# Kernel optimization log

Measured on AMD Instinct MI355X. Metric: run time of the kernel, lower is better.

Reference implementation:

```python
import jax, jax.numpy as jnp
import numpy as np

B, L, HID, NH = 1, 2048, 3072, 24
HD = HID // NH          # 128
MLP = HID * 4           # 12288


def _layernorm(x, eps=1e-6):
    # LayerNorm without affine (pre_norm)
    mu = jnp.mean(x, axis=-1, keepdims=True)
    var = jnp.mean(jnp.square(x - mu), axis=-1, keepdims=True)
    return (x - mu) * jax.lax.rsqrt(var + eps)


def _rmsnorm(x, w):
    # torch.nn.RMSNorm with eps=None -> finfo(dtype).eps
    eps = jnp.finfo(x.dtype).eps
    ms = jnp.mean(jnp.square(x), axis=-1, keepdims=True)
    return x * jax.lax.rsqrt(ms + eps) * w


def _apply_rope(x, pe):
    # x: (B, L, H, D); pe: (B, 1, L, D//2, 2, 2)
    b, l, h, d = x.shape
    x_ = x.astype(jnp.float32).reshape(b, l, h, d // 2, 1, 2)
    f = pe[:, :, :, None]                       # (B,1,L,1,D//2,2,2)
    out = f[..., 0] * x_[..., 0] + f[..., 1] * x_[..., 1]
    return out.reshape(b, l, h, d).astype(x.dtype)


def setup_inputs() -> dict:
    key = jax.random.key(0)
    ks = jax.random.split(key, 16)
    s = 0.02
    # pe as proper 2x2 rotation matrices (EmbedND output structure)
    theta = jax.random.uniform(ks[0], (L, HD // 2), minval=0.0, maxval=2.0 * np.pi)
    cos, sin = jnp.cos(theta), jnp.sin(theta)
    rot = jnp.stack([jnp.stack([cos, -sin], -1), jnp.stack([sin, cos], -1)], -2)
    pe = rot[None, None].astype(jnp.float32)    # (1,1,L,HD//2,2,2)
    rnd = lambda k, shp: jax.random.normal(k, shp, jnp.float32)
    return {
        "x": rnd(ks[1], (B, L, HID)),
        "vec": rnd(ks[2], (B, HID)),
        "pe": pe,
        "w_mod": rnd(ks[3], (HID, 3 * HID)) * s,
        "b_mod": rnd(ks[4], (3 * HID,)) * s,
        "w_qkv": rnd(ks[5], (HID, 3 * HID)) * s,
        "b_qkv": rnd(ks[6], (3 * HID,)) * s,
        "w_fc1": rnd(ks[7], (HID, MLP)) * s,
        "b_fc1": rnd(ks[8], (MLP,)) * s,
        "w_fc2": rnd(ks[9], (MLP, HID)) * s,
        "b_fc2": rnd(ks[10], (HID,)) * s,
        "w_out": rnd(ks[11], (HID, HID)) * s,
        "b_out": rnd(ks[12], (HID,)) * s,
        "norm_q_w": jnp.ones((HD,), jnp.float32),
        "norm_k_w": jnp.ones((HD,), jnp.float32),
    }


def reference(x, vec, pe, w_mod, b_mod, w_qkv, b_qkv, w_fc1, b_fc1,
              w_fc2, b_fc2, w_out, b_out, norm_q_w, norm_k_w):
    # modulation: AWQ linear on silu(vec)
    mod = jax.nn.silu(vec) @ w_mod + b_mod            # (B, 3*HID)
    shift, scale, gate = jnp.split(mod[:, None, :], 3, axis=-1)
    x_mod = _layernorm(x) * (1.0 + scale) + shift      # (B, L, HID)

    # qkv projection (SVDQ linear, dequantized math == dense GEMM)
    qkv = x_mod @ w_qkv + b_qkv
    q, k, v = jnp.split(qkv, 3, axis=-1)
    q = _rmsnorm(q.reshape(B, L, NH, HD), norm_q_w)
    k = _rmsnorm(k.reshape(B, L, NH, HD), norm_k_w)
    q = _apply_rope(q, pe)
    k = _apply_rope(k, pe)
    v = v.reshape(B, L, NH, HD)

    # scaled dot-product attention
    scores = jnp.einsum("blhd,bmhd->bhlm", q, k) / jnp.sqrt(jnp.float32(HD))
    probs = jax.nn.softmax(scores, axis=-1)
    attn = jnp.einsum("bhlm,bmhd->blhd", probs, v).reshape(B, L, HID)

    # parallel MLP branch
    mlp = jax.nn.gelu(x_mod @ w_fc1 + b_fc1, approximate=True)
    mlp = mlp @ w_fc2 + b_fc2

    out = attn @ w_out + b_out + mlp
    return x + gate * out
```

## Files before the change

kernel.cpp:

```cpp
#include <hip/hip_runtime.h>
#include <hip/hip_bf16.h>
#include <stdint.h>


typedef __bf16 bf16;
typedef bf16 bf16x2 __attribute__((ext_vector_type(2)));
typedef bf16 bf16x4 __attribute__((ext_vector_type(4)));
typedef bf16 bf16x8 __attribute__((ext_vector_type(8)));
typedef float f32x4 __attribute__((ext_vector_type(4)));

#define L_SEQ 2048
#define HIDD  3072
#define NHH   24
#define HDD   128
#define MLPD  12288
#define N3Q   9216

struct PB { bf16* p[8]; };

__device__ __forceinline__ void gload_lds16(const bf16* g, bf16* l) {
  __builtin_amdgcn_global_load_lds(
      (const __attribute__((address_space(1))) unsigned int*)g,
      (__attribute__((address_space(3))) unsigned int*)l, 16, 0, 0);
}

__device__ __forceinline__ float gelu_tanh(float x) {
  float z = 0.7978845608028654f * (x + 0.044715f * x * x * x);
  float t = 1.f - 2.f / (__expf(2.f * z) + 1.f);
  return 0.5f * x * (1.f + t);
}

__global__ __launch_bounds__(256) void mod_partial(
    const float* __restrict__ vec, const float* __restrict__ w_mod,
    float* __restrict__ part) {
  __shared__ float sv[256];
  int y = blockIdx.y;
  int i0 = y * 256;
  {
    float xv = vec[i0 + threadIdx.x];
    sv[threadIdx.x] = xv / (1.f + __expf(-xv));
  }
  __syncthreads();
  int j = blockIdx.x * 256 + threadIdx.x;
  float acc = 0.f;
#pragma unroll 8
  for (int i = 0; i < 256; ++i)
    acc += sv[i] * w_mod[(size_t)(i0 + i) * N3Q + j];
  part[y * N3Q + j] = acc;
}

__global__ __launch_bounds__(256) void mod_reduce(
    const float* __restrict__ part, const float* __restrict__ b_mod,
    float* __restrict__ mod) {
  int j = blockIdx.x * 256 + threadIdx.x;
  float s = b_mod[j];
#pragma unroll
  for (int p = 0; p < 12; ++p) s += part[p * N3Q + j];
  mod[j] = s;
}

__global__ __launch_bounds__(256) void ln_mod_k(
    const float* __restrict__ x, const float* __restrict__ mod,
    bf16* __restrict__ xm) {
  __shared__ float sb[4];
  int l = blockIdx.x, t = threadIdx.x;
  const float* xr = x + (size_t)l * HIDD;
  float4 v[3];
  float s = 0.f;
#pragma unroll
  for (int p = 0; p < 3; ++p) {
    v[p] = *(const float4*)(xr + p * 1024 + t * 4);
    s += v[p].x + v[p].y + v[p].z + v[p].w;
  }
#pragma unroll
  for (int o = 32; o >= 1; o >>= 1) s += __shfl_xor(s, o);
  if (!(t & 63)) sb[t >> 6] = s;
  __syncthreads();
  float mean = (sb[0] + sb[1] + sb[2] + sb[3]) * (1.f / HIDD);
  __syncthreads();
  float vs = 0.f;
#pragma unroll
  for (int p = 0; p < 3; ++p) {
    float a = v[p].x - mean, b = v[p].y - mean, c = v[p].z - mean,
          d = v[p].w - mean;
    vs += a * a + b * b + c * c + d * d;
  }
#pragma unroll
  for (int o = 32; o >= 1; o >>= 1) vs += __shfl_xor(vs, o);
  if (!(t & 63)) sb[t >> 6] = vs;
  __syncthreads();
  float var = (sb[0] + sb[1] + sb[2] + sb[3]) * (1.f / HIDD);
  float rs = rsqrtf(var + 1e-6f);
#pragma unroll
  for (int p = 0; p < 3; ++p) {
    int j = p * 1024 + t * 4;
    float4 sc = *(const float4*)(mod + HIDD + j);
    float4 sh = *(const float4*)(mod + j);
    bf16x4 o;
    o[0] = (bf16)((v[p].x - mean) * rs * (1.f + sc.x) + sh.x);
    o[1] = (bf16)((v[p].y - mean) * rs * (1.f + sc.y) + sh.y);
    o[2] = (bf16)((v[p].z - mean) * rs * (1.f + sc.z) + sh.z);
    o[3] = (bf16)((v[p].w - mean) * rs * (1.f + sc.w) + sh.w);
    *(bf16x4*)(xm + (size_t)l * HIDD + j) = o;
  }
}

__global__ __launch_bounds__(256) void convT(
    const float* __restrict__ src, bf16* __restrict__ dst, int K, int N) {
  __shared__ bf16 tl[64 * 72];
  int n0 = blockIdx.x * 64, k0 = blockIdx.y * 64;
  int t = threadIdx.x;
#pragma unroll
  for (int p = 0; p < 4; ++p) {
    int idx = p * 256 + t;
    int kr = idx >> 4, c4 = (idx & 15) << 2;
    float4 v = *(const float4*)(src + (size_t)(k0 + kr) * N + n0 + c4);
    bf16x4 b;
    b[0] = (bf16)v.x; b[1] = (bf16)v.y; b[2] = (bf16)v.z; b[3] = (bf16)v.w;
    *(bf16x4*)(tl + kr * 72 + c4) = b;
  }
  __syncthreads();
#pragma unroll
  for (int p = 0; p < 2; ++p) {
    int idx = p * 256 + t;
    int nr = idx >> 3, c = idx & 7;
    bf16x8 o;
#pragma unroll
    for (int j = 0; j < 8; ++j) o[j] = tl[(c * 8 + j) * 72 + nr];
    *(bf16x8*)(dst + (size_t)(n0 + nr) * K + k0 + c * 8) = o;
  }
}

template <int EPI>
__global__ __launch_bounds__(512, 2) void gemm256(
    const bf16* __restrict__ A, const bf16* __restrict__ BT,
    const float* __restrict__ bias, int lda, int klen, int ldc, int gy,
    int gz, PB dst, bf16* __restrict__ o1) {
  __shared__ bf16 LA[2][2][8192];
  __shared__ bf16 LB[2][2][8192];
  const int tid = threadIdx.x;
  const int w = tid >> 6, lane = tid & 63;
  const int wm = w >> 2, wn = w & 3;
  const int g = lane >> 4, r16 = lane & 15;
  const int hb = wn >> 1, brow = (wn & 1) * 64;

  const int nwg = 8 * gy * gz;
  int id = (int)blockIdx.x;
  int sw = (id & 7) * (nwg >> 3) + (id >> 3);
  const int bx = sw & 7;
  const int rem = sw >> 3;
  const int by = rem % gy;
  const int bz = rem / gy;

  const int row0 = bx * 256, col0 = by * 256;
  const size_t kb = (size_t)bz * klen;

  const int s_r = tid >> 3, s_c = tid & 7;
  const bf16* gA = A + (size_t)(row0 + s_r) * lda + kb + ((s_c ^ (s_r & 7)) << 3);
  const bf16* gB = BT + (size_t)(col0 + s_r) * lda + kb + ((s_c ^ (s_r & 7)) << 3);
  const int wofs = w * 512;

#define STG_A(buf, h, t)                                                       \
  do {                                                                         \
    gload_lds16(gA + (size_t)((h) * 128) * lda + (size_t)(t) * 64,             \
                &LA[buf][h][wofs]);                                            \
    gload_lds16(gA + (size_t)((h) * 128 + 64) * lda + (size_t)(t) * 64,        \
                &LA[buf][h][4096 + wofs]);                                     \
  } while (0)
#define STG_B(buf, h, t)                                                       \
  do {                                                                         \
    gload_lds16(gB + (size_t)((h) * 128) * lda + (size_t)(t) * 64,             \
                &LB[buf][h][wofs]);                                            \
    gload_lds16(gB + (size_t)((h) * 128 + 64) * lda + (size_t)(t) * 64,        \
                &LB[buf][h][4096 + wofs]);                                     \
  } while (0)
#define LGKM0()                                               \
  do {                                                        \
    asm volatile("s_waitcnt lgkmcnt(0)" ::: "memory");        \
    __builtin_amdgcn_sched_barrier(0);                        \
  } while (0)
#define RD_A4(DST, LAP, MB)                                                    \
  _Pragma("unroll") for (int m_ = 0; m_ < 4; ++m_)                             \
  _Pragma("unroll") for (int kk_ = 0; kk_ < 2; ++kk_)                          \
      DST[m_][kk_] = *(const bf16x8*)((LAP) + (((MB) + m_) * 16 + r16) * 64 +  \
                                      (((kk_ * 4 + g) ^ (r16 & 7)) << 3));
#define RD_B2(DST, LBP, NB)                                                    \
  _Pragma("unroll") for (int n_ = 0; n_ < 2; ++n_)                             \
  _Pragma("unroll") for (int kk_ = 0; kk_ < 2; ++kk_)                          \
      DST[n_][kk_] = *(const bf16x8*)(                                         \
          (LBP) + (brow + ((NB) + n_) * 16 + r16) * 64 +                       \
          (((kk_ * 4 + g) ^ (r16 & 7)) << 3));
#define QUAD(AF, BF, MB, NB)                                                   \
  do {                                                                         \
    __builtin_amdgcn_s_setprio(1);                                             \
    _Pragma("unroll") for (int kk_ = 0; kk_ < 2; ++kk_)                        \
    _Pragma("unroll") for (int m_ = 0; m_ < 4; ++m_)                           \
    _Pragma("unroll") for (int n_ = 0; n_ < 2; ++n_)                           \
        acc[(MB) + m_][(NB) + n_] = __builtin_amdgcn_mfma_f32_16x16x32_bf16(   \
            AF[m_][kk_], BF[n_][kk_], acc[(MB) + m_][(NB) + n_], 0, 0, 0);     \
    __builtin_amdgcn_s_setprio(0);                                             \
  } while (0)

#define GROUP(TB, T1, T2)                                                      \
  do {                                                                         \
    const bf16* la = &LA[TB][wm][0];                                           \
    const bf16* lb = &LB[TB][hb][0];                                           \
    bf16x8 aL[4][2], aH[4][2], bL[2][2], bH[2][2];                             \
                                           \
    RD_A4(aL, la, 0);                                                          \
    RD_B2(bL, lb, 0);                                                          \
    if ((T1) < nk) STG_B(TB ^ 1, 1, T1);                                       \
    asm volatile("s_waitcnt lgkmcnt(8)" ::: "memory");                         \
    __builtin_amdgcn_s_barrier();                                              \
    LGKM0();                                                                   \
    QUAD(aL, bL, 0, 0);                                                        \
    __builtin_amdgcn_s_barrier();                                              \
                      \
    RD_A4(aH, la, 4);                                                          \
    __builtin_amdgcn_s_barrier();                                              \
    LGKM0();                                                                   \
    QUAD(aH, bL, 4, 0);                                                        \
    __builtin_amdgcn_s_barrier();                                              \
     \
    RD_B2(bH, lb, 2);                                                          \
    if ((T2) < nk) { STG_A(TB, 0, T2); STG_A(TB, 1, T2); }                     \
    __builtin_amdgcn_s_barrier();                                              \
    LGKM0();                                                                   \
    QUAD(aL, bH, 0, 2);                                                        \
    __builtin_amdgcn_s_barrier();                                              \
       \
    if ((T2) < nk) {                                                           \
      STG_B(TB, 0, T2);                                                        \
      asm volatile("s_waitcnt vmcnt(6)" ::: "memory");                         \
    } else {                                                                   \
      asm volatile("s_waitcnt vmcnt(0)" ::: "memory");                         \
    }                                                                          \
    __builtin_amdgcn_s_barrier();                                              \
    QUAD(aH, bH, 4, 2);                                                        \
    __builtin_amdgcn_s_barrier();                                              \
  } while (0)

  f32x4 acc[8][4] = {};
  const int nk = klen >> 6;

  STG_A(0, 0, 0); STG_A(0, 1, 0); STG_B(0, 0, 0); STG_B(0, 1, 0);
  STG_A(1, 0, 1); STG_A(1, 1, 1); STG_B(1, 0, 1);
  asm volatile("s_waitcnt vmcnt(6)" ::: "memory");
  __builtin_amdgcn_s_barrier();

  for (int t = 0; t < nk; t += 2) {
    GROUP(0, t + 1, t + 2);
    GROUP(1, t + 2, t + 3);
  }
#undef STG_A
#undef STG_B
#undef LGKM0
#undef RD_A4
#undef RD_B2
#undef QUAD
#undef GROUP

  bf16* dp = (EPI == 0) ? dst.p[bz] : o1;
#pragma unroll
  for (int m = 0; m < 8; ++m) {
    int row = row0 + wm * 128 + m * 16 + g * 4;
#pragma unroll
    for (int n = 0; n < 4; ++n) {
      int col = col0 + wn * 64 + n * 16 + r16;
      float bv = (EPI == 1) ? bias[col] : 0.f;
#pragma unroll
      for (int r = 0; r < 4; ++r) {
        float v = acc[m][n][r] + bv;
        if (EPI == 1) v = gelu_tanh(v);
        dp[(size_t)(row + r) * ldc + col] = (bf16)v;
      }
    }
  }
}

__global__ __launch_bounds__(256) void qknorm_rope_k(
    const bf16* __restrict__ P0, const bf16* __restrict__ P1,
    const float* __restrict__ b_qkv, const float* __restrict__ pe,
    const float* __restrict__ qw, const float* __restrict__ kw,
    bf16* __restrict__ qb, bf16* __restrict__ kb) {
  int t = threadIdx.x, lane = t & 63, w = t >> 6;
  int pair = blockIdx.x * 4 + w;
  int h = pair % NHH, l = pair / NHH;
  size_t qi = (size_t)l * N3Q + h * HDD + 2 * lane;
  size_t ob = (size_t)l * HIDD + h * HDD + 2 * lane;
  float4 f = *(const float4*)(pe + (size_t)l * 256 + lane * 4);
  float2 wq = *(const float2*)(qw + 2 * lane);
  float2 wk = *(const float2*)(kw + 2 * lane);
  {
    bf16x2 a = *(const bf16x2*)(P0 + qi);
    bf16x2 b = *(const bf16x2*)(P1 + qi);
    float2 bq = *(const float2*)(b_qkv + h * HDD + 2 * lane);
    float x0 = (float)a[0] + (float)b[0] + bq.x;
    float x1 = (float)a[1] + (float)b[1] + bq.y;
    float ss = x0 * x0 + x1 * x1;
#pragma unroll
    for (int o = 32; o >= 1; o >>= 1) ss += __shfl_xor(ss, o);
    float rs = rsqrtf(ss * (1.f / HDD) + 1.1920929e-7f);
    x0 *= rs * wq.x; x1 *= rs * wq.y;
    const float qs = 0.08838834764831845f;
    bf16x2 ov;
    ov[0] = (bf16)((f.x * x0 + f.y * x1) * qs);
    ov[1] = (bf16)((f.z * x0 + f.w * x1) * qs);
    *(bf16x2*)(qb + ob) = ov;
  }
  {
    bf16x2 a = *(const bf16x2*)(P0 + qi + HIDD);
    bf16x2 b = *(const bf16x2*)(P1 + qi + HIDD);
    float2 bk = *(const float2*)(b_qkv + HIDD + h * HDD + 2 * lane);
    float x0 = (float)a[0] + (float)b[0] + bk.x;
    float x1 = (float)a[1] + (float)b[1] + bk.y;
    float ss = x0 * x0 + x1 * x1;
#pragma unroll
    for (int o = 32; o >= 1; o >>= 1) ss += __shfl_xor(ss, o);
    float rs = rsqrtf(ss * (1.f / HDD) + 1.1920929e-7f);
    x0 *= rs * wk.x; x1 *= rs * wk.y;
    bf16x2 ov;
    ov[0] = (bf16)(f.x * x0 + f.y * x1);
    ov[1] = (bf16)(f.z * x0 + f.w * x1);
    *(bf16x2*)(kb + ob) = ov;
  }
}

__global__ __launch_bounds__(256) void vtrans_k(
    const bf16* __restrict__ P0, const bf16* __restrict__ P1,
    const float* __restrict__ b_qkv, bf16* __restrict__ vt) {
  __shared__ bf16 tl[128 * 128];
  int t = threadIdx.x, lt = blockIdx.x, h = blockIdx.y;
#pragma unroll
  for (int p = 0; p < 8; ++p) {
    int idx = p * 256 + t;
    int i = idx >> 4, c = idx & 15;
    size_t gi = (size_t)(lt * 128 + i) * N3Q + 2 * HIDD + h * HDD + c * 8;
    bf16x8 a = *(const bf16x8*)(P0 + gi);
    bf16x8 b = *(const bf16x8*)(P1 + gi);
    bf16x8 val;
#pragma unroll
    for (int e = 0; e < 8; ++e)
      val[e] = (bf16)((float)a[e] + (float)b[e] +
                      b_qkv[2 * HIDD + h * HDD + c * 8 + e]);
    *(bf16x8*)(tl + i * 128 + ((c ^ (i & 15)) << 3)) = val;
  }
  __syncthreads();
#pragma unroll
  for (int p = 0; p < 8; ++p) {
    int idx = p * 256 + t;
    int j = idx >> 4, i8 = (idx & 15) << 3;
    bf16x8 o;
#pragma unroll
    for (int e = 0; e < 8; ++e) {
      int row = i8 + e;
      o[e] = tl[row * 128 + ((((j >> 3) ^ (row & 15)) << 3) | (j & 7))];
    }
    *(bf16x8*)(vt + ((size_t)h * HDD + j) * L_SEQ + lt * 128 + i8) = o;
  }
}

__global__ __launch_bounds__(256) void attn_k(
    const bf16* __restrict__ q, const bf16* __restrict__ k,
    const bf16* __restrict__ vt, bf16* __restrict__ out) {
  __shared__ bf16 Ks[64 * 128];
  __shared__ bf16 Vs[128 * 64];
  __shared__ bf16 Ps[4][16 * 72];
  int tid = threadIdx.x, lane = tid & 63, w = tid >> 6;
  int g = lane >> 4, r16 = lane & 15;
  int qt = blockIdx.x, h = blockIdx.y;
  int qbase = qt * 64 + w * 16;

  bf16x8 qreg[4];
  const bf16* qrow = q + (size_t)(qbase + r16) * HIDD + h * HDD;
#pragma unroll
  for (int c = 0; c < 4; ++c) qreg[c] = *(const bf16x8*)(qrow + c * 32 + g * 8);

  f32x4 acc[8] = {};
  float m_run = -3.0e38f, l_run = 0.f;
  bf16* ps = &Ps[w][0];

  for (int kv0 = 0; kv0 < L_SEQ; kv0 += 64) {
    __syncthreads();
#pragma unroll
    for (int p = 0; p < 4; ++p) {
      int ci = p * 256 + tid;
      {
        int rr = ci >> 4, cc = ci & 15;
        gload_lds16(k + (size_t)(kv0 + rr) * HIDD + h * HDD +
                        ((cc ^ (rr & 15)) << 3),
                    Ks + ((p * 4 + w) << 9));
      }
      {
        int rr = ci >> 3, cc = ci & 7;
        gload_lds16(vt + ((size_t)h * HDD + rr) * L_SEQ + kv0 +
                        ((cc ^ (rr & 7)) << 3),
                    Vs + ((p * 4 + w) << 9));
      }
    }
    __syncthreads();

    f32x4 st[4] = {};
#pragma unroll
    for (int m4 = 0; m4 < 4; ++m4) {
#pragma unroll
      for (int c = 0; c < 4; ++c) {
        int rr = m4 * 16 + r16;
        bf16x8 kf =
            *(const bf16x8*)(Ks + rr * 128 + (((c * 4 + g) ^ (rr & 15)) << 3));
        st[m4] =
            __builtin_amdgcn_mfma_f32_16x16x32_bf16(kf, qreg[c], st[m4], 0, 0, 0);
      }
    }
    float cmax = -3.0e38f;
#pragma unroll
    for (int m4 = 0; m4 < 4; ++m4)
#pragma unroll
      for (int r = 0; r < 4; ++r) cmax = fmaxf(cmax, st[m4][r]);
    cmax = fmaxf(cmax, __shfl_xor(cmax, 16));
    cmax = fmaxf(cmax, __shfl_xor(cmax, 32));
    float m_new = fmaxf(m_run, cmax);
    float corr = __expf(m_run - m_new);
    float psum = 0.f;
#pragma unroll
    for (int m4 = 0; m4 < 4; ++m4) {
      bf16x4 pk;
#pragma unroll
      for (int r = 0; r < 4; ++r) {
        float pv = __expf(st[m4][r] - m_new);
        psum += pv;
        pk[r] = (bf16)pv;
      }
      *(bf16x4*)(ps + r16 * 72 + m4 * 16 + g * 4) = pk;
    }
    psum += __shfl_xor(psum, 16);
    psum += __shfl_xor(psum, 32);
    l_run = l_run * corr + psum;
    m_run = m_new;
    float corr_r[4];
#pragma unroll
    for (int r = 0; r < 4; ++r) corr_r[r] = __shfl(corr, g * 4 + r);
#pragma unroll
    for (int nt = 0; nt < 8; ++nt)
#pragma unroll
      for (int r = 0; r < 4; ++r) acc[nt][r] *= corr_r[r];
#pragma unroll
    for (int ks = 0; ks < 2; ++ks) {
      bf16x8 pf = *(const bf16x8*)(ps + r16 * 72 + ks * 32 + g * 8);
#pragma unroll
      for (int nt = 0; nt < 8; ++nt) {
        int rr = nt * 16 + r16;
        bf16x8 vf =
            *(const bf16x8*)(Vs + rr * 64 + (((ks * 4 + g) ^ (rr & 7)) << 3));
        acc[nt] = __builtin_amdgcn_mfma_f32_16x16x32_bf16(pf, vf, acc[nt], 0, 0, 0);
      }
    }
  }
  float inv = 1.f / l_run;
  float inv_r[4];
#pragma unroll
  for (int r = 0; r < 4; ++r) inv_r[r] = __shfl(inv, g * 4 + r);
#pragma unroll
  for (int nt = 0; nt < 8; ++nt)
#pragma unroll
    for (int r = 0; r < 4; ++r)
      out[(size_t)(qbase + g * 4 + r) * HIDD + h * HDD + nt * 16 + r16] =
          (bf16)(acc[nt][r] * inv_r[r]);
}

__global__ __launch_bounds__(256) void osum_k(
    const bf16* __restrict__ a, const bf16* __restrict__ b,
    const bf16* __restrict__ c, const bf16* __restrict__ d,
    float* __restrict__ o) {
  size_t i = ((size_t)blockIdx.x * 256 + threadIdx.x) * 4;
  bf16x4 va = *(const bf16x4*)(a + i);
  bf16x4 vb = *(const bf16x4*)(b + i);
  bf16x4 vc = *(const bf16x4*)(c + i);
  bf16x4 vd = *(const bf16x4*)(d + i);
  float4 s;
  s.x = (float)va[0] + (float)vb[0] + (float)vc[0] + (float)vd[0];
  s.y = (float)va[1] + (float)vb[1] + (float)vc[1] + (float)vd[1];
  s.z = (float)va[2] + (float)vb[2] + (float)vc[2] + (float)vd[2];
  s.w = (float)va[3] + (float)vb[3] + (float)vc[3] + (float)vd[3];
  *(float4*)(o + i) = s;
}

__global__ __launch_bounds__(256) void final_k(
    const float* __restrict__ x, PB ps, const float* __restrict__ mod,
    const float* __restrict__ b_out, const float* __restrict__ b_fc2,
    float* __restrict__ out) {
  int l = blockIdx.x, t = threadIdx.x;
#pragma unroll
  for (int p = 0; p < 3; ++p) {
    int c = p * 1024 + t * 4;
    size_t idx = (size_t)l * HIDD + c;
    float4 xv = *(const float4*)(x + idx);
    float4 gv = *(const float4*)(mod + 2 * HIDD + c);
    float4 bo = *(const float4*)(b_out + c);
    float4 bf = *(const float4*)(b_fc2 + c);
    float4 da = *(const float4*)(out + idx);
    float a0 = da.x + bo.x + bf.x, a1 = da.y + bo.y + bf.y;
    float a2 = da.z + bo.z + bf.z, a3 = da.w + bo.w + bf.w;
#pragma unroll
    for (int i = 0; i < 8; ++i) {
      bf16x4 v = *(const bf16x4*)(ps.p[i] + idx);
      a0 += (float)v[0]; a1 += (float)v[1];
      a2 += (float)v[2]; a3 += (float)v[3];
    }
    float4 o;
    o.x = xv.x + gv.x * a0;
    o.y = xv.y + gv.y * a1;
    o.z = xv.z + gv.z * a2;
    o.w = xv.w + gv.w * a3;
    *(float4*)(out + idx) = o;
  }
}

extern "C" void kernel_launch(void* const* d_in, const int* in_sizes, int n_in,
                              void* d_out, int out_size, void* d_ws,
                              size_t ws_size, hipStream_t stream) {
  const float* x     = (const float*)d_in[0];
  const float* vec   = (const float*)d_in[1];
  const float* pe    = (const float*)d_in[2];
  const float* w_mod = (const float*)d_in[3];
  const float* b_mod = (const float*)d_in[4];
  const float* w_qkv = (const float*)d_in[5];
  const float* b_qkv = (const float*)d_in[6];
  const float* w_fc1 = (const float*)d_in[7];
  const float* b_fc1 = (const float*)d_in[8];
  const float* w_fc2 = (const float*)d_in[9];
  const float* b_fc2 = (const float*)d_in[10];
  const float* w_out = (const float*)d_in[11];
  const float* b_out = (const float*)d_in[12];
  const float* qw    = (const float*)d_in[13];
  const float* kw    = (const float*)d_in[14];
  float* out = (float*)d_out;

  char* ws = (char*)d_ws;
  float* mod  = (float*)(ws + 0);
  bf16* xmod  = (bf16*)(ws + 65536);
  bf16* qb    = (bf16*)(ws + 12648448);
  bf16* kbuf  = (bf16*)(ws + 25231360);
  bf16* vt    = (bf16*)(ws + 37814272);
  bf16* att   = (bf16*)(ws + 50397184);
  bf16* mlpF  = (bf16*)(ws + 62980096);
  bf16* wt    = (bf16*)(ws + 113311744);
  bf16* P0    = (bf16*)(ws + 188809216);
  float* part = (float*)(ws + 188809216);
  bf16* P1    = mlpF;
  bf16* H1    = (bf16*)(ws + 188809216 + 12582912);
  bf16* H2    = (bf16*)(ws + 188809216 + 25165824);
  PB Z = {};

  mod_partial<<<dim3(36, 12), 256, 0, stream>>>(vec, w_mod, part);
  mod_reduce<<<36, 256, 0, stream>>>(part, b_mod, mod);
  ln_mod_k<<<2048, 256, 0, stream>>>(x, mod, xmod);

  convT<<<dim3(144, 48), 256, 0, stream>>>(w_qkv, wt, 3072, 9216);
  PB Pq = {}; Pq.p[0] = P0; Pq.p[1] = P1;
  gemm256<0><<<576, 512, 0, stream>>>(xmod, wt, nullptr, 3072, 1536, 9216, 36,
                                      2, Pq, nullptr);
  qknorm_rope_k<<<12288, 256, 0, stream>>>(P0, P1, b_qkv, pe, qw, kw, qb, kbuf);
  vtrans_k<<<dim3(16, 24), 256, 0, stream>>>(P0, P1, b_qkv, vt);
  attn_k<<<dim3(32, 24), 256, 0, stream>>>(qb, kbuf, vt, att);

  convT<<<dim3(48, 48), 256, 0, stream>>>(w_out, wt, 3072, 3072);
  PB Po = {}; Po.p[0] = qb; Po.p[1] = kbuf; Po.p[2] = vt; Po.p[3] = P0;
  gemm256<0><<<384, 512, 0, stream>>>(att, wt, nullptr, 3072, 768, 3072, 12, 4,
                                      Po, nullptr);
  osum_k<<<6144, 256, 0, stream>>>(qb, kbuf, vt, P0, out);

  convT<<<dim3(192, 48), 256, 0, stream>>>(w_fc1, wt, 3072, 12288);
  gemm256<1><<<384, 512, 0, stream>>>(xmod, wt, b_fc1, 3072, 3072, 12288, 48,
                                      1, Z, mlpF);

  convT<<<dim3(48, 192), 256, 0, stream>>>(w_fc2, wt, 12288, 3072);
  PB Pf = {};
  Pf.p[0] = xmod; Pf.p[1] = qb; Pf.p[2] = kbuf; Pf.p[3] = vt;
  Pf.p[4] = att;  Pf.p[5] = P0; Pf.p[6] = H1;   Pf.p[7] = H2;
  gemm256<0><<<768, 512, 0, stream>>>(mlpF, wt, nullptr, 12288, 1536, 3072, 12,
                                      8, Pf, nullptr);

  final_k<<<2048, 256, 0, stream>>>(x, Pf, mod, b_out, b_fc2, out);
}
```

Baseline: 876.2 us.

## Software-pipeline LDS fragment reads in GEMM and split-K the fc1 GEMM

Restructures the GEMM inner GROUP so that each fragment's LDS reads are issued one quad ahead, including prefetching the next tile's A-low fragment, and drops several barriers and lgkm waits. The goal is to hide LDS latency behind MFMA work. Separately, fc1 now runs as a 2-way split-K GEMM writing bf16 partials, followed by a new elementwise kernel that sums the partials, adds the bias and applies GELU. This doubles the grid to fill the GPU, at the cost of extra partial-buffer traffic, one more launch, and bf16 rounding of the partials before the sum.

```diff
diff --git a/kernel.cpp b/kernel.cpp
--- a/kernel.cpp
+++ b/kernel.cpp
@@ -179,6 +179,7 @@
     asm volatile("s_waitcnt lgkmcnt(0)" ::: "memory");        \
     __builtin_amdgcn_sched_barrier(0);                        \
   } while (0)
+#define SB0() __builtin_amdgcn_sched_barrier(0)
 #define RD_A4(DST, LAP, MB)                                                    \
   _Pragma("unroll") for (int m_ = 0; m_ < 4; ++m_)                             \
   _Pragma("unroll") for (int kk_ = 0; kk_ < 2; ++kk_)                          \
@@ -205,48 +206,50 @@
   do {                                                                         \
     const bf16* la = &LA[TB][wm][0];                                           \
     const bf16* lb = &LB[TB][hb][0];                                           \
-    bf16x8 aL[4][2], aH[4][2], bL[2][2], bH[2][2];                             \
-                                           \
-    RD_A4(aL, la, 0);                                                          \
+    const bf16* laN = &LA[TB ^ 1][wm][0];                                      \
+          \
+    LGKM0();                                                                   \
+    if ((T1) < nk) STG_B(TB ^ 1, 1, T1);                                       \
     RD_B2(bL, lb, 0);                                                          \
-    if ((T1) < nk) STG_B(TB ^ 1, 1, T1);                                       \
-    asm volatile("s_waitcnt lgkmcnt(8)" ::: "memory");                         \
-    __builtin_amdgcn_s_barrier();                                              \
-    LGKM0();                                                                   \
+    RD_A4(aH, la, 4);                                                          \
+    SB0();                                                                     \
     QUAD(aL, bL, 0, 0);                                                        \
     __builtin_amdgcn_s_barrier();                                              \
-                      \
-    RD_A4(aH, la, 4);                                                          \
-    __builtin_amdgcn_s_barrier();                                              \
+                                               \
     LGKM0();                                                                   \
+    RD_B2(bH, lb, 2);                                                          \
+    SB0();                                                                     \
     QUAD(aH, bL, 4, 0);                                                        \
     __builtin_amdgcn_s_barrier();                                              \
-     \
-    RD_B2(bH, lb, 2);                                                          \
-    if ((T2) < nk) { STG_A(TB, 0, T2); STG_A(TB, 1, T2); }                     \
-    __builtin_amdgcn_s_barrier();                                              \
+         \
     LGKM0();                                                                   \
-    QUAD(aL, bH, 0, 2);                                                        \
-    __builtin_amdgcn_s_barrier();                                              \
-       \
     if ((T2) < nk) {                                                           \
-      STG_B(TB, 0, T2);                                                        \
-      asm volatile("s_waitcnt vmcnt(6)" ::: "memory");                         \
+      STG_A(TB, 0, T2);                                                        \
+      STG_A(TB, 1, T2);                                                        \
+      asm volatile("s_waitcnt vmcnt(4)" ::: "memory");                         \
     } else {                                                                   \
       asm volatile("s_waitcnt vmcnt(0)" ::: "memory");                         \
     }                                                                          \
+    SB0();                                                                     \
+    QUAD(aL, bH, 0, 2);                                                        \
     __builtin_amdgcn_s_barrier();                                              \
+          \
+    if ((T2) < nk) STG_B(TB, 0, T2);                                           \
+    if ((T1) < nk) { RD_A4(aL, laN, 0); }                                      \
+    SB0();                                                                     \
     QUAD(aH, bH, 4, 2);                                                        \
     __builtin_amdgcn_s_barrier();                                              \
   } while (0)
 
   f32x4 acc[8][4] = {};
+  bf16x8 aL[4][2], aH[4][2], bL[2][2], bH[2][2];
   const int nk = klen >> 6;
 
   STG_A(0, 0, 0); STG_A(0, 1, 0); STG_B(0, 0, 0); STG_B(0, 1, 0);
   STG_A(1, 0, 1); STG_A(1, 1, 1); STG_B(1, 0, 1);
   asm volatile("s_waitcnt vmcnt(6)" ::: "memory");
   __builtin_amdgcn_s_barrier();
+  { const bf16* la0 = &LA[0][wm][0]; RD_A4(aL, la0, 0); }
 
   for (int t = 0; t < nk; t += 2) {
     GROUP(0, t + 1, t + 2);
@@ -255,6 +258,7 @@
 #undef STG_A
 #undef STG_B
 #undef LGKM0
+#undef SB0
 #undef RD_A4
 #undef RD_B2
 #undef QUAD
@@ -485,6 +489,23 @@
   *(float4*)(o + i) = s;
 }
 
+__global__ __launch_bounds__(256) void sumgelu_k(
+    const bf16* __restrict__ p0, const bf16* __restrict__ p1,
+    const float* __restrict__ b, bf16* __restrict__ o) {
+  size_t i = ((size_t)blockIdx.x * 256 + threadIdx.x) * 8;
+  int col = (int)(i % MLPD);
+  bf16x8 a = *(const bf16x8*)(p0 + i);
+  bf16x8 c = *(const bf16x8*)(p1 + i);
+  float4 b0 = *(const float4*)(b + col);
+  float4 b1 = *(const float4*)(b + col + 4);
+  float bb[8] = {b0.x, b0.y, b0.z, b0.w, b1.x, b1.y, b1.z, b1.w};
+  bf16x8 o8;
+#pragma unroll
+  for (int j = 0; j < 8; ++j)
+    o8[j] = (bf16)gelu_tanh((float)a[j] + (float)c[j] + bb[j]);
+  *(bf16x8*)(o + i) = o8;
+}
+
 __global__ __launch_bounds__(256) void final_k(
     const float* __restrict__ x, PB ps, const float* __restrict__ mod,
     const float* __restrict__ b_out, const float* __restrict__ b_fc2,
@@ -571,8 +592,10 @@
   osum_k<<<6144, 256, 0, stream>>>(qb, kbuf, vt, P0, out);
 
   convT<<<dim3(192, 48), 256, 0, stream>>>(w_fc1, wt, 3072, 12288);
-  gemm256<1><<<384, 512, 0, stream>>>(xmod, wt, b_fc1, 3072, 3072, 12288, 48,
-                                      1, Z, mlpF);
+  PB Pg = {}; Pg.p[0] = mlpF; Pg.p[1] = qb;
+  gemm256<0><<<768, 512, 0, stream>>>(xmod, wt, nullptr, 3072, 1536, 12288, 48,
+                                      2, Pg, nullptr);
+  sumgelu_k<<<12288, 256, 0, stream>>>(mlpF, qb, b_fc1, mlpF);
 
   convT<<<dim3(48, 192), 256, 0, stream>>>(w_fc2, wt, 12288, 3072);
   PB Pf = {};
```

New measurement: 1.136 ms. 1.3x slower.

## Fuse QKV and FC1 GEMMs into one launch without split-K

Applied to the files above, without the earlier changes.

Merges the QKV projection and the FC1+GELU projection, which share the same xmod input, into a single GEMM launch over a concatenated output width. Each tile picks its transposed weight source and epilogue based on its column block. The QKV part no longer uses split-K, so qknorm and vtrans read one partial buffer instead of summing two. Transposed weights are staged in reused scratch (the q buffer and the output buffer), which ties correctness to buffer lifetimes and gives a larger single grid with full-K tiles.

```diff
diff --git a/kernel.cpp b/kernel.cpp
--- a/kernel.cpp
+++ b/kernel.cpp
@@ -135,7 +135,8 @@
 __global__ __launch_bounds__(512, 2) void gemm256(
     const bf16* __restrict__ A, const bf16* __restrict__ BT,
     const float* __restrict__ bias, int lda, int klen, int ldc, int gy,
-    int gz, PB dst, bf16* __restrict__ o1) {
+    int gz, PB dst, const bf16* __restrict__ BT2,
+    const bf16* __restrict__ BT3) {
   __shared__ bf16 LA[2][2][8192];
   __shared__ bf16 LB[2][2][8192];
   const int tid = threadIdx.x;
@@ -157,7 +158,14 @@
 
   const int s_r = tid >> 3, s_c = tid & 7;
   const bf16* gA = A + (size_t)(row0 + s_r) * lda + kb + ((s_c ^ (s_r & 7)) << 3);
-  const bf16* gB = BT + (size_t)(col0 + s_r) * lda + kb + ((s_c ^ (s_r & 7)) << 3);
+  const bf16* bbase = BT;
+  int bcol = col0;
+  if (EPI == 2) {
+    if (by >= 36)      { bbase = BT3; bcol = col0 - 9216; }
+    else if (by >= 32) { bbase = BT2; bcol = col0 - 8192; }
+  }
+  const bf16* gB =
+      bbase + (size_t)(bcol + s_r) * lda + kb + ((s_c ^ (s_r & 7)) << 3);
   const int wofs = w * 512;
 
 #define STG_A(buf, h, t)                                                       \
@@ -260,29 +268,54 @@
 #undef QUAD
 #undef GROUP
 
-  bf16* dp = (EPI == 0) ? dst.p[bz] : o1;
-#pragma unroll
-  for (int m = 0; m < 8; ++m) {
-    int row = row0 + wm * 128 + m * 16 + g * 4;
-#pragma unroll
-    for (int n = 0; n < 4; ++n) {
-      int col = col0 + wn * 64 + n * 16 + r16;
-      float bv = (EPI == 1) ? bias[col] : 0.f;
-#pragma unroll
-      for (int r = 0; r < 4; ++r) {
-        float v = acc[m][n][r] + bv;
-        if (EPI == 1) v = gelu_tanh(v);
-        dp[(size_t)(row + r) * ldc + col] = (bf16)v;
+  if (EPI == 2 && by < 36) {
+    bf16* dp = dst.p[0];
+#pragma unroll
+    for (int m = 0; m < 8; ++m) {
+      int row = row0 + wm * 128 + m * 16 + g * 4;
+#pragma unroll
+      for (int n = 0; n < 4; ++n) {
+        int col = col0 + wn * 64 + n * 16 + r16;
+#pragma unroll
+        for (int r = 0; r < 4; ++r)
+          dp[(size_t)(row + r) * N3Q + col] = (bf16)acc[m][n][r];
+      }
+    }
+  } else if (EPI == 2) {
+    bf16* dp = dst.p[1];
+#pragma unroll
+    for (int m = 0; m < 8; ++m) {
+      int row = row0 + wm * 128 + m * 16 + g * 4;
+#pragma unroll
+      for (int n = 0; n < 4; ++n) {
+        int col = col0 - 9216 + wn * 64 + n * 16 + r16;
+        float bv = bias[col];
+#pragma unroll
+        for (int r = 0; r < 4; ++r)
+          dp[(size_t)(row + r) * MLPD + col] = (bf16)gelu_tanh(acc[m][n][r] + bv);
+      }
+    }
+  } else {
+    bf16* dp = dst.p[bz];
+#pragma unroll
+    for (int m = 0; m < 8; ++m) {
+      int row = row0 + wm * 128 + m * 16 + g * 4;
+#pragma unroll
+      for (int n = 0; n < 4; ++n) {
+        int col = col0 + wn * 64 + n * 16 + r16;
+#pragma unroll
+        for (int r = 0; r < 4; ++r)
+          dp[(size_t)(row + r) * ldc + col] = (bf16)acc[m][n][r];
       }
     }
   }
 }
 
 __global__ __launch_bounds__(256) void qknorm_rope_k(
-    const bf16* __restrict__ P0, const bf16* __restrict__ P1,
-    const float* __restrict__ b_qkv, const float* __restrict__ pe,
-    const float* __restrict__ qw, const float* __restrict__ kw,
-    bf16* __restrict__ qb, bf16* __restrict__ kb) {
+    const bf16* __restrict__ P, const float* __restrict__ b_qkv,
+    const float* __restrict__ pe, const float* __restrict__ qw,
+    const float* __restrict__ kw, bf16* __restrict__ qb,
+    bf16* __restrict__ kb) {
   int t = threadIdx.x, lane = t & 63, w = t >> 6;
   int pair = blockIdx.x * 4 + w;
   int h = pair % NHH, l = pair / NHH;
@@ -292,11 +325,10 @@
   float2 wq = *(const float2*)(qw + 2 * lane);
   float2 wk = *(const float2*)(kw + 2 * lane);
   {
-    bf16x2 a = *(const bf16x2*)(P0 + qi);
-    bf16x2 b = *(const bf16x2*)(P1 + qi);
+    bf16x2 a = *(const bf16x2*)(P + qi);
     float2 bq = *(const float2*)(b_qkv + h * HDD + 2 * lane);
-    float x0 = (float)a[0] + (float)b[0] + bq.x;
-    float x1 = (float)a[1] + (float)b[1] + bq.y;
+    float x0 = (float)a[0] + bq.x;
+    float x1 = (float)a[1] + bq.y;
     float ss = x0 * x0 + x1 * x1;
 #pragma unroll
     for (int o = 32; o >= 1; o >>= 1) ss += __shfl_xor(ss, o);
@@ -309,11 +341,10 @@
     *(bf16x2*)(qb + ob) = ov;
   }
   {
-    bf16x2 a = *(const bf16x2*)(P0 + qi + HIDD);
-    bf16x2 b = *(const bf16x2*)(P1 + qi + HIDD);
+    bf16x2 a = *(const bf16x2*)(P + qi + HIDD);
     float2 bk = *(const float2*)(b_qkv + HIDD + h * HDD + 2 * lane);
-    float x0 = (float)a[0] + (float)b[0] + bk.x;
-    float x1 = (float)a[1] + (float)b[1] + bk.y;
+    float x0 = (float)a[0] + bk.x;
+    float x1 = (float)a[1] + bk.y;
     float ss = x0 * x0 + x1 * x1;
 #pragma unroll
     for (int o = 32; o >= 1; o >>= 1) ss += __shfl_xor(ss, o);
@@ -327,8 +358,8 @@
 }
 
 __global__ __launch_bounds__(256) void vtrans_k(
-    const bf16* __restrict__ P0, const bf16* __restrict__ P1,
-    const float* __restrict__ b_qkv, bf16* __restrict__ vt) {
+    const bf16* __restrict__ P, const float* __restrict__ b_qkv,
+    bf16* __restrict__ vt) {
   __shared__ bf16 tl[128 * 128];
   int t = threadIdx.x, lt = blockIdx.x, h = blockIdx.y;
 #pragma unroll
@@ -336,13 +367,11 @@
     int idx = p * 256 + t;
     int i = idx >> 4, c = idx & 15;
     size_t gi = (size_t)(lt * 128 + i) * N3Q + 2 * HIDD + h * HDD + c * 8;
-    bf16x8 a = *(const bf16x8*)(P0 + gi);
-    bf16x8 b = *(const bf16x8*)(P1 + gi);
+    bf16x8 a = *(const bf16x8*)(P + gi);
     bf16x8 val;
 #pragma unroll
     for (int e = 0; e < 8; ++e)
-      val[e] = (bf16)((float)a[e] + (float)b[e] +
-                      b_qkv[2 * HIDD + h * HDD + c * 8 + e]);
+      val[e] = (bf16)((float)a[e] + b_qkv[2 * HIDD + h * HDD + c * 8 + e]);
     *(bf16x8*)(tl + i * 128 + ((c ^ (i & 15)) << 3)) = val;
   }
   __syncthreads();
@@ -547,39 +576,39 @@
   bf16* wt    = (bf16*)(ws + 113311744);
   bf16* P0    = (bf16*)(ws + 188809216);
   float* part = (float*)(ws + 188809216);
-  bf16* P1    = mlpF;
   bf16* H1    = (bf16*)(ws + 188809216 + 12582912);
   bf16* H2    = (bf16*)(ws + 188809216 + 25165824);
+  bf16* wtQlo = qb;
+  bf16* wtScr = (bf16*)out;
   PB Z = {};
 
   mod_partial<<<dim3(36, 12), 256, 0, stream>>>(vec, w_mod, part);
   mod_reduce<<<36, 256, 0, stream>>>(part, b_mod, mod);
   ln_mod_k<<<2048, 256, 0, stream>>>(x, mod, xmod);
 
-  convT<<<dim3(144, 48), 256, 0, stream>>>(w_qkv, wt, 3072, 9216);
-  PB Pq = {}; Pq.p[0] = P0; Pq.p[1] = P1;
-  gemm256<0><<<576, 512, 0, stream>>>(xmod, wt, nullptr, 3072, 1536, 9216, 36,
-                                      2, Pq, nullptr);
-  qknorm_rope_k<<<12288, 256, 0, stream>>>(P0, P1, b_qkv, pe, qw, kw, qb, kbuf);
-  vtrans_k<<<dim3(16, 24), 256, 0, stream>>>(P0, P1, b_qkv, vt);
+  convT<<<dim3(128, 48), 256, 0, stream>>>(w_qkv, wtQlo, 3072, 9216);
+  convT<<<dim3(16, 48), 256, 0, stream>>>(w_qkv + 8192, wtScr, 3072, 9216);
+  convT<<<dim3(192, 48), 256, 0, stream>>>(w_fc1, wt, 3072, 12288);
+  PB Pc = {}; Pc.p[0] = P0; Pc.p[1] = mlpF;
+  gemm256<2><<<672, 512, 0, stream>>>(xmod, wtQlo, b_fc1, 3072, 3072, 0, 84,
+                                      1, Pc, wtScr, wt);
+
+  qknorm_rope_k<<<12288, 256, 0, stream>>>(P0, b_qkv, pe, qw, kw, qb, kbuf);
+  vtrans_k<<<dim3(16, 24), 256, 0, stream>>>(P0, b_qkv, vt);
   attn_k<<<dim3(32, 24), 256, 0, stream>>>(qb, kbuf, vt, att);
 
   convT<<<dim3(48, 48), 256, 0, stream>>>(w_out, wt, 3072, 3072);
   PB Po = {}; Po.p[0] = qb; Po.p[1] = kbuf; Po.p[2] = vt; Po.p[3] = P0;
   gemm256<0><<<384, 512, 0, stream>>>(att, wt, nullptr, 3072, 768, 3072, 12, 4,
-                                      Po, nullptr);
+                                      Po, nullptr, nullptr);
   osum_k<<<6144, 256, 0, stream>>>(qb, kbuf, vt, P0, out);
-
-  convT<<<dim3(192, 48), 256, 0, stream>>>(w_fc1, wt, 3072, 12288);
-  gemm256<1><<<384, 512, 0, stream>>>(xmod, wt, b_fc1, 3072, 3072, 12288, 48,
-                                      1, Z, mlpF);
 
   convT<<<dim3(48, 192), 256, 0, stream>>>(w_fc2, wt, 12288, 3072);
   PB Pf = {};
   Pf.p[0] = xmod; Pf.p[1] = qb; Pf.p[2] = kbuf; Pf.p[3] = vt;
   Pf.p[4] = att;  Pf.p[5] = P0; Pf.p[6] = H1;   Pf.p[7] = H2;
   gemm256<0><<<768, 512, 0, stream>>>(mlpF, wt, nullptr, 12288, 1536, 3072, 12,
-                                      8, Pf, nullptr);
+                                      8, Pf, nullptr, nullptr);
 
   final_k<<<2048, 256, 0, stream>>>(x, Pf, mod, b_out, b_fc2, out);
 }
```

Result: faster. 848.7 us (-3.1%).
